# Optimization experiments

Measured on AMD Instinct MI355X. Metric: run time of the kernel, lower is better.

## Reference

```python
import jax, jax.numpy as jnp
import numpy as np

DIM = 1024
HEADS = 16
DIM_HEADS = DIM // HEADS  # 64
DIM_HIDDEN = DIM_HEADS * HEADS


def setup_inputs() -> dict:
    key = jax.random.key(0)
    k1, k2, k3, k4, k5 = jax.random.split(key, 5)
    b, t = 2, 2048
    x = jax.random.normal(k1, (b, t, DIM), dtype=jnp.float32)
    # torch nn.Linear weights are [out_features, in_features]
    s = DIM ** -0.5
    W_q = jax.random.normal(k2, (DIM_HIDDEN, DIM), dtype=jnp.float32) * s
    W_kv = jax.random.normal(k3, (2 * DIM_HIDDEN, DIM), dtype=jnp.float32) * s
    W_out = jax.random.normal(k4, (DIM, DIM_HIDDEN), dtype=jnp.float32) * s
    b_out = jax.random.normal(k5, (DIM,), dtype=jnp.float32) * 0.01
    return {"x": x, "W_q": W_q, "W_kv": W_kv, "W_out": W_out, "b_out": b_out}


def reference(x, W_q, W_kv, W_out, b_out):
    b, t, d = x.shape
    h, e = HEADS, DIM_HEADS
    # projections (Linear: x @ W.T)
    q = jnp.einsum('btd,fd->btf', x, W_q)
    kv = jnp.einsum('btd,fd->btf', x, W_kv)
    k, v = jnp.split(kv, 2, axis=-1)
    # split heads -> (b, h, t, e)
    split = lambda z: z.reshape(b, t, h, e).transpose(0, 2, 1, 3)
    q, k, v = split(q), split(k), split(v)
    # scaled dot-product attention; original uses exp/sum/div softmax
    scores = jnp.einsum('bhqe,bhke->bhqk', q, k) * (e ** -0.5)
    attn = jax.nn.softmax(scores, axis=-1)
    out = jnp.einsum('bhqk,bhke->bhqe', attn, v)
    out = out.transpose(0, 2, 1, 3).reshape(b, t, h * e)
    return jnp.einsum('btf,df->btd', out, W_out) + b_out
```

## Files before the change

kernel.cpp:

```cpp
#include <hip/hip_runtime.h>
#include <hip/hip_bf16.h>

#define BB   2
#define TT   2048
#define DD   1024
#define HH   16
#define EE   64
#define BT   4096

typedef __attribute__((ext_vector_type(8))) short bf16x8;
typedef __attribute__((ext_vector_type(4))) float floatx4;

__device__ __forceinline__ unsigned short f2bf(float f) {
  unsigned int x = __float_as_uint(f);
  x += 0x7fffu + ((x >> 16) & 1u);
  return (unsigned short)(x >> 16);
}
__device__ __forceinline__ uint4 pack8(const float4& a, const float4& b) {
  union { uint4 u; __hip_bfloat162 h[4]; } r;
  r.h[0] = __float22bfloat162_rn(make_float2(a.x, a.y));
  r.h[1] = __float22bfloat162_rn(make_float2(a.z, a.w));
  r.h[2] = __float22bfloat162_rn(make_float2(b.x, b.y));
  r.h[3] = __float22bfloat162_rn(make_float2(b.z, b.w));
  return r.u;
}
__device__ __forceinline__ void ld16(unsigned short* lds, const unsigned short* g) {
  __builtin_amdgcn_global_load_lds(
      (const __attribute__((address_space(1))) unsigned int*)g,
      (__attribute__((address_space(3))) unsigned int*)lds, 16, 0, 0);
}

#define GX   524288
#define GWQ  131072
#define GWKV 262144
#define GWO  131072

__global__ __launch_bounds__(256) void convert_kernel(
    const float* __restrict__ X,  const float* __restrict__ Wq,
    const float* __restrict__ Wkv, const float* __restrict__ Wout,
    unsigned short* __restrict__ Xb, unsigned short* __restrict__ Wb,
    unsigned short* __restrict__ Wob) {
  int g = blockIdx.x * 256 + threadIdx.x;
  const float* src; unsigned short* dst; int gi;
  if (g < GX)                        { src = X;    dst = Xb;  gi = g; }
  else if ((g -= GX) < GWQ)          { src = Wq;   dst = Wb;  gi = g; }
  else if ((g -= GWQ) < GWKV)        { src = Wkv;  dst = Wb + (size_t)GWQ * 8; gi = g; }
  else                               { src = Wout; dst = Wob; gi = g - GWKV; }
  const float4* s4 = reinterpret_cast<const float4*>(src) + (size_t)gi * 2;
  float4 a = s4[0], b = s4[1];
  reinterpret_cast<uint4*>(dst)[gi] = pack8(a, b);
}

__global__ __launch_bounds__(256) void gemm_qkv_mfma(
    const unsigned short* __restrict__ Xb,
    const unsigned short* __restrict__ Wb,
    unsigned short* __restrict__ Qh,
    unsigned short* __restrict__ Kh,
    unsigned short* __restrict__ Vt) {
  __shared__ __align__(16) unsigned short As[128 * 64];
  __shared__ __align__(16) unsigned short Bs[128 * 64];
  const int tid  = threadIdx.x;
  const int lane = tid & 63, w = tid >> 6;
  const int wm = w >> 1, wn = w & 1;
  const int q = lane >> 4, c = lane & 15;
  const int bm0 = blockIdx.y * 128;
  const int bn0 = blockIdx.x * 128;
  const unsigned short* Ag = Xb + (size_t)bm0 * DD;
  const unsigned short* Bg = Wb + (size_t)bn0 * DD;

  floatx4 acc[4][4];
#pragma unroll
  for (int i = 0; i < 4; ++i)
#pragma unroll
    for (int j = 0; j < 4; ++j) acc[i][j] = (floatx4){0.f, 0.f, 0.f, 0.f};

  int prow[4], pch[4];
#pragma unroll
  for (int t = 0; t < 4; ++t) {
    int s = (w * 4 + t) * 64 + lane;
    prow[t] = s >> 3;
    pch[t]  = (s & 7) ^ (prow[t] & 7);
  }
  int aoff[4][2], boff[4][2];
#pragma unroll
  for (int i = 0; i < 4; ++i)
#pragma unroll
    for (int h = 0; h < 2; ++h) {
      aoff[i][h] = (wm * 64 + i * 16 + c) * 64 + (((q + h * 4) ^ (c & 7)) << 3);
      boff[i][h] = (wn * 64 + i * 16 + c) * 64 + (((q + h * 4) ^ (c & 7)) << 3);
    }

  for (int kk = 0; kk < DD; kk += 64) {
    __syncthreads();
#pragma unroll
    for (int t = 0; t < 4; ++t) {
      int i = w * 4 + t;
      ld16(&As[i * 512], &Ag[(size_t)prow[t] * DD + kk + pch[t] * 8]);
      ld16(&Bs[i * 512], &Bg[(size_t)prow[t] * DD + kk + pch[t] * 8]);
    }
    __syncthreads();
    bf16x8 af[4][2], bfr[4][2];
#pragma unroll
    for (int i = 0; i < 4; ++i)
#pragma unroll
      for (int h = 0; h < 2; ++h) {
        af[i][h]  = *reinterpret_cast<const bf16x8*>(&As[aoff[i][h]]);
        bfr[i][h] = *reinterpret_cast<const bf16x8*>(&Bs[boff[i][h]]);
      }
#pragma unroll
    for (int i = 0; i < 4; ++i)
#pragma unroll
      for (int j = 0; j < 4; ++j) {
        acc[i][j] = __builtin_amdgcn_mfma_f32_16x16x32_bf16(af[i][0], bfr[j][0], acc[i][j], 0, 0, 0);
        acc[i][j] = __builtin_amdgcn_mfma_f32_16x16x32_bf16(af[i][1], bfr[j][1], acc[i][j], 0, 0, 0);
      }
  }

  const int region = bn0 >> 10;
#pragma unroll
  for (int i = 0; i < 4; ++i) {
#pragma unroll
    for (int j = 0; j < 4; ++j) {
#pragma unroll
      for (int reg = 0; reg < 4; ++reg) {
        int m = bm0 + wm * 64 + i * 16 + q * 4 + reg;
        int n = bn0 + wn * 64 + j * 16 + c;
        int nb = n & 1023;
        int h = nb >> 6, e = nb & 63;
        int b = m >> 11, t = m & 2047;
        unsigned short v = f2bf(acc[i][j][reg]);
        if (region == 0)      Qh[((size_t)((b * HH + h) * TT + t)) * EE + e] = v;
        else if (region == 1) Kh[((size_t)((b * HH + h) * TT + t)) * EE + e] = v;
        else                  Vt[((size_t)(b * HH + h)) * EE * TT + (size_t)e * TT + t] = v;
      }
    }
  }
}

#define LP 72

__global__ __launch_bounds__(256) void attn_kernel(
    const unsigned short* __restrict__ Qh,
    const unsigned short* __restrict__ Kh,
    const unsigned short* __restrict__ Vtg,
    unsigned short* __restrict__ Aw) {
  __shared__ __align__(16) unsigned short Qs[64 * LP];
  __shared__ __align__(16) unsigned short Ks[64 * LP];
  __shared__ __align__(16) unsigned short Vs[64 * LP];
  __shared__ __align__(16) unsigned short Ps[64 * LP];

  const int tid  = threadIdx.x;
  const int lane = tid & 63;
  const int w    = tid >> 6;
  const int q    = lane >> 4;
  const int c    = lane & 15;
  const int rbase = w * 16;

  const int qt = blockIdx.x;
  const int bh = blockIdx.y;
  const size_t base = (size_t)bh * TT * EE;
  const unsigned short* Qp = Qh + base + (size_t)qt * 64 * EE;
  const unsigned short* Kp = Kh + base;
  const unsigned short* Vp = Vtg + base;

#pragma unroll
  for (int s = 0; s < 2; ++s) {
    int o = tid + s * 256;
    int r = o >> 3, e0 = (o & 7) << 3;
    *reinterpret_cast<uint4*>(&Qs[r * LP + e0]) =
        *reinterpret_cast<const uint4*>(&Qp[(size_t)r * EE + e0]);
  }

  float l_r[4] = {0.f, 0.f, 0.f, 0.f};
  floatx4 o_acc[4];
#pragma unroll
  for (int nt = 0; nt < 4; ++nt) o_acc[nt] = (floatx4){0.f, 0.f, 0.f, 0.f};

  const int a_off = (rbase + c) * LP + q * 8;
  const int b_off = c * LP + q * 8;
  const int p_off = (rbase + q * 4) * LP + c;

  for (int kt = 0; kt < TT / 64; ++kt) {
    __syncthreads();
#pragma unroll
    for (int s = 0; s < 2; ++s) {
      int o = tid + s * 256;
      int r = o >> 3, x0 = (o & 7) << 3;
      *reinterpret_cast<uint4*>(&Ks[r * LP + x0]) =
          *reinterpret_cast<const uint4*>(&Kp[(size_t)(kt * 64 + r) * EE + x0]);
      *reinterpret_cast<uint4*>(&Vs[r * LP + x0]) =
          *reinterpret_cast<const uint4*>(&Vp[(size_t)r * TT + kt * 64 + x0]);
    }
    __syncthreads();

    floatx4 sacc[4];
#pragma unroll
    for (int nt = 0; nt < 4; ++nt) sacc[nt] = (floatx4){0.f, 0.f, 0.f, 0.f};
    bf16x8 aq0 = *reinterpret_cast<const bf16x8*>(&Qs[a_off]);
    bf16x8 aq1 = *reinterpret_cast<const bf16x8*>(&Qs[a_off + 32]);
#pragma unroll
    for (int nt = 0; nt < 4; ++nt) {
      bf16x8 bk0 = *reinterpret_cast<const bf16x8*>(&Ks[b_off + nt * 16 * LP]);
      bf16x8 bk1 = *reinterpret_cast<const bf16x8*>(&Ks[b_off + nt * 16 * LP + 32]);
      sacc[nt] = __builtin_amdgcn_mfma_f32_16x16x32_bf16(aq0, bk0, sacc[nt], 0, 0, 0);
      sacc[nt] = __builtin_amdgcn_mfma_f32_16x16x32_bf16(aq1, bk1, sacc[nt], 0, 0, 0);
    }

#pragma unroll
    for (int nt = 0; nt < 4; ++nt)
#pragma unroll
      for (int reg = 0; reg < 4; ++reg) {
        float p = __expf(sacc[nt][reg] * 0.125f);
        l_r[reg] += p;
        Ps[p_off + reg * LP + nt * 16] = f2bf(p);
      }

    __syncthreads();

    bf16x8 ap0 = *reinterpret_cast<const bf16x8*>(&Ps[a_off]);
    bf16x8 ap1 = *reinterpret_cast<const bf16x8*>(&Ps[a_off + 32]);
#pragma unroll
    for (int nt = 0; nt < 4; ++nt) {
      bf16x8 bv0 = *reinterpret_cast<const bf16x8*>(&Vs[b_off + nt * 16 * LP]);
      bf16x8 bv1 = *reinterpret_cast<const bf16x8*>(&Vs[b_off + nt * 16 * LP + 32]);
      o_acc[nt] = __builtin_amdgcn_mfma_f32_16x16x32_bf16(ap0, bv0, o_acc[nt], 0, 0, 0);
      o_acc[nt] = __builtin_amdgcn_mfma_f32_16x16x32_bf16(ap1, bv1, o_acc[nt], 0, 0, 0);
    }
  }

#pragma unroll
  for (int reg = 0; reg < 4; ++reg)
#pragma unroll
    for (int mask = 1; mask < 16; mask <<= 1)
      l_r[reg] += __shfl_xor(l_r[reg], mask, 64);

  const int b = bh >> 4, h = bh & 15;
#pragma unroll
  for (int reg = 0; reg < 4; ++reg) {
    int t = qt * 64 + rbase + q * 4 + reg;
    float inv = 1.0f / l_r[reg];
    size_t rowoff = ((size_t)(b * TT + t)) * DD + h * EE;
#pragma unroll
    for (int nt = 0; nt < 4; ++nt)
      Aw[rowoff + nt * 16 + c] = f2bf(o_acc[nt][reg] * inv);
  }
}

__global__ __launch_bounds__(256) void gemm_out_mfma(
    const unsigned short* __restrict__ A,
    const unsigned short* __restrict__ Wob,
    const float* __restrict__ bias,
    float* __restrict__ out) {
  __shared__ __align__(16) unsigned short As[128 * 64];
  __shared__ __align__(16) unsigned short Bs[64 * 64];
  const int tid  = threadIdx.x;
  const int lane = tid & 63, w = tid >> 6;
  const int wm = w >> 1, wn = w & 1;
  const int q = lane >> 4, c = lane & 15;
  const int bm0 = blockIdx.y * 128;
  const int bn0 = blockIdx.x * 64;
  const unsigned short* Ag = A + (size_t)bm0 * DD;
  const unsigned short* Bg = Wob + (size_t)bn0 * DD;

  floatx4 acc[4][2];
#pragma unroll
  for (int i = 0; i < 4; ++i)
#pragma unroll
    for (int j = 0; j < 2; ++j) acc[i][j] = (floatx4){0.f, 0.f, 0.f, 0.f};

  int parow[4], pach[4];
#pragma unroll
  for (int t = 0; t < 4; ++t) {
    int s = (w * 4 + t) * 64 + lane;
    parow[t] = s >> 3;
    pach[t]  = (s & 7) ^ (parow[t] & 7);
  }
  int pbrow[2], pbch[2];
#pragma unroll
  for (int t = 0; t < 2; ++t) {
    int s = (w * 2 + t) * 64 + lane;
    pbrow[t] = s >> 3;
    pbch[t]  = (s & 7) ^ (pbrow[t] & 7);
  }

  for (int kk = 0; kk < DD; kk += 64) {
    __syncthreads();
#pragma unroll
    for (int t = 0; t < 4; ++t)
      ld16(&As[(w * 4 + t) * 512], &Ag[(size_t)parow[t] * DD + kk + pach[t] * 8]);
#pragma unroll
    for (int t = 0; t < 2; ++t)
      ld16(&Bs[(w * 2 + t) * 512], &Bg[(size_t)pbrow[t] * DD + kk + pbch[t] * 8]);
    __syncthreads();
    bf16x8 af[4][2], bfr[2][2];
#pragma unroll
    for (int h = 0; h < 2; ++h) {
      int ksw = ((q + h * 4) ^ (c & 7)) << 3;
#pragma unroll
      for (int i = 0; i < 4; ++i)
        af[i][h] = *reinterpret_cast<const bf16x8*>(&As[(wm * 64 + i * 16 + c) * 64 + ksw]);
#pragma unroll
      for (int j = 0; j < 2; ++j)
        bfr[j][h] = *reinterpret_cast<const bf16x8*>(&Bs[(wn * 32 + j * 16 + c) * 64 + ksw]);
    }
#pragma unroll
    for (int i = 0; i < 4; ++i)
#pragma unroll
      for (int j = 0; j < 2; ++j) {
        acc[i][j] = __builtin_amdgcn_mfma_f32_16x16x32_bf16(af[i][0], bfr[j][0], acc[i][j], 0, 0, 0);
        acc[i][j] = __builtin_amdgcn_mfma_f32_16x16x32_bf16(af[i][1], bfr[j][1], acc[i][j], 0, 0, 0);
      }
  }

#pragma unroll
  for (int i = 0; i < 4; ++i) {
#pragma unroll
    for (int j = 0; j < 2; ++j) {
      int n = bn0 + wn * 32 + j * 16 + c;
      float bv = bias[n];
#pragma unroll
      for (int reg = 0; reg < 4; ++reg) {
        int m = bm0 + wm * 64 + i * 16 + q * 4 + reg;
        out[(size_t)m * DD + n] = acc[i][j][reg] + bv;
      }
    }
  }
}

extern "C" void kernel_launch(void* const* d_in, const int* in_sizes, int n_in,
                              void* d_out, int out_size, void* d_ws, size_t ws_size,
                              hipStream_t stream) {
  const float* X    = (const float*)d_in[0];
  const float* Wq   = (const float*)d_in[1];
  const float* Wkv  = (const float*)d_in[2];
  const float* Wout = (const float*)d_in[3];
  const float* bout = (const float*)d_in[4];
  float* out = (float*)d_out;

  unsigned short* Qh  = (unsigned short*)d_ws;
  unsigned short* Kh  = Qh + (size_t)BT * DD;
  unsigned short* Vt  = Kh + (size_t)BT * DD;
  unsigned short* Aw  = Vt + (size_t)BT * DD;
  unsigned short* Xb  = Aw;
  unsigned short* Wb  = Aw + (size_t)BT * DD;
  unsigned short* Wob = Wb + (size_t)3 * 1024 * DD;

  convert_kernel<<<dim3(4096), 256, 0, stream>>>(X, Wq, Wkv, Wout, Xb, Wb, Wob);
  gemm_qkv_mfma<<<dim3(24, 32), 256, 0, stream>>>(Xb, Wb, Qh, Kh, Vt);
  attn_kernel<<<dim3(32, 32), 256, 0, stream>>>(Qh, Kh, Vt, Aw);
  gemm_out_mfma<<<dim3(16, 32), 256, 0, stream>>>(Aw, Wob, bout, out);
}
```

Baseline: 232.3 us.

## Transpose S via swapped MFMA operands, reuse Q LDS for P, fold scale into projection

```diff
diff --git a/kernel.cpp b/kernel.cpp
--- a/kernel.cpp
+++ b/kernel.cpp
@@ -15,6 +15,11 @@
   unsigned int x = __float_as_uint(f);
   x += 0x7fffu + ((x >> 16) & 1u);
   return (unsigned short)(x >> 16);
+}
+__device__ __forceinline__ unsigned int pack2u(float a, float b) {
+  union { __hip_bfloat162 h; unsigned int u; } r;
+  r.h = __float22bfloat162_rn(make_float2(a, b));
+  return r.u;
 }
 __device__ __forceinline__ uint4 pack8(const float4& a, const float4& b) {
   union { uint4 u; __hip_bfloat162 h[4]; } r;
@@ -117,6 +122,7 @@
   }
 
   const int region = bn0 >> 10;
+  const float scl = (region == 0) ? 0.125f : 1.0f;
 #pragma unroll
   for (int i = 0; i < 4; ++i) {
 #pragma unroll
@@ -128,7 +134,7 @@
         int nb = n & 1023;
         int h = nb >> 6, e = nb & 63;
         int b = m >> 11, t = m & 2047;
-        unsigned short v = f2bf(acc[i][j][reg]);
+        unsigned short v = f2bf(acc[i][j][reg] * scl);
         if (region == 0)      Qh[((size_t)((b * HH + h) * TT + t)) * EE + e] = v;
         else if (region == 1) Kh[((size_t)((b * HH + h) * TT + t)) * EE + e] = v;
         else                  Vt[((size_t)(b * HH + h)) * EE * TT + (size_t)e * TT + t] = v;
@@ -147,7 +153,6 @@
   __shared__ __align__(16) unsigned short Qs[64 * LP];
   __shared__ __align__(16) unsigned short Ks[64 * LP];
   __shared__ __align__(16) unsigned short Vs[64 * LP];
-  __shared__ __align__(16) unsigned short Ps[64 * LP];
 
   const int tid  = threadIdx.x;
   const int lane = tid & 63;
@@ -170,15 +175,17 @@
     *reinterpret_cast<uint4*>(&Qs[r * LP + e0]) =
         *reinterpret_cast<const uint4*>(&Qp[(size_t)r * EE + e0]);
   }
-
-  float l_r[4] = {0.f, 0.f, 0.f, 0.f};
-  floatx4 o_acc[4];
-#pragma unroll
-  for (int nt = 0; nt < 4; ++nt) o_acc[nt] = (floatx4){0.f, 0.f, 0.f, 0.f};
+  __syncthreads();
 
   const int a_off = (rbase + c) * LP + q * 8;
   const int b_off = c * LP + q * 8;
-  const int p_off = (rbase + q * 4) * LP + c;
+  const bf16x8 aq0 = *reinterpret_cast<const bf16x8*>(&Qs[a_off]);
+  const bf16x8 aq1 = *reinterpret_cast<const bf16x8*>(&Qs[a_off + 32]);
+
+  float l_sum = 0.0f;
+  floatx4 o_acc[4];
+#pragma unroll
+  for (int nt = 0; nt < 4; ++nt) o_acc[nt] = (floatx4){0.f, 0.f, 0.f, 0.f};
 
   for (int kt = 0; kt < TT / 64; ++kt) {
     __syncthreads();
@@ -195,30 +202,30 @@
 
     floatx4 sacc[4];
 #pragma unroll
-    for (int nt = 0; nt < 4; ++nt) sacc[nt] = (floatx4){0.f, 0.f, 0.f, 0.f};
-    bf16x8 aq0 = *reinterpret_cast<const bf16x8*>(&Qs[a_off]);
-    bf16x8 aq1 = *reinterpret_cast<const bf16x8*>(&Qs[a_off + 32]);
-#pragma unroll
     for (int nt = 0; nt < 4; ++nt) {
       bf16x8 bk0 = *reinterpret_cast<const bf16x8*>(&Ks[b_off + nt * 16 * LP]);
       bf16x8 bk1 = *reinterpret_cast<const bf16x8*>(&Ks[b_off + nt * 16 * LP + 32]);
-      sacc[nt] = __builtin_amdgcn_mfma_f32_16x16x32_bf16(aq0, bk0, sacc[nt], 0, 0, 0);
-      sacc[nt] = __builtin_amdgcn_mfma_f32_16x16x32_bf16(aq1, bk1, sacc[nt], 0, 0, 0);
-    }
-
-#pragma unroll
-    for (int nt = 0; nt < 4; ++nt)
-#pragma unroll
-      for (int reg = 0; reg < 4; ++reg) {
-        float p = __expf(sacc[nt][reg] * 0.125f);
-        l_r[reg] += p;
-        Ps[p_off + reg * LP + nt * 16] = f2bf(p);
-      }
-
-    __syncthreads();
-
-    bf16x8 ap0 = *reinterpret_cast<const bf16x8*>(&Ps[a_off]);
-    bf16x8 ap1 = *reinterpret_cast<const bf16x8*>(&Ps[a_off + 32]);
+      sacc[nt] = (floatx4){0.f, 0.f, 0.f, 0.f};
+      sacc[nt] = __builtin_amdgcn_mfma_f32_16x16x32_bf16(bk0, aq0, sacc[nt], 0, 0, 0);
+      sacc[nt] = __builtin_amdgcn_mfma_f32_16x16x32_bf16(bk1, aq1, sacc[nt], 0, 0, 0);
+    }
+
+#pragma unroll
+    for (int nt = 0; nt < 4; ++nt) {
+      float p0 = __expf(sacc[nt][0]);
+      float p1 = __expf(sacc[nt][1]);
+      float p2 = __expf(sacc[nt][2]);
+      float p3 = __expf(sacc[nt][3]);
+      l_sum += (p0 + p1) + (p2 + p3);
+      uint2 pk;
+      pk.x = pack2u(p0, p1);
+      pk.y = pack2u(p2, p3);
+      *reinterpret_cast<uint2*>(&Qs[(rbase + c) * LP + nt * 16 + q * 4]) = pk;
+    }
+    asm volatile("s_waitcnt lgkmcnt(0)" ::: "memory");
+
+    bf16x8 ap0 = *reinterpret_cast<const bf16x8*>(&Qs[a_off]);
+    bf16x8 ap1 = *reinterpret_cast<const bf16x8*>(&Qs[a_off + 32]);
 #pragma unroll
     for (int nt = 0; nt < 4; ++nt) {
       bf16x8 bv0 = *reinterpret_cast<const bf16x8*>(&Vs[b_off + nt * 16 * LP]);
@@ -228,21 +235,21 @@
     }
   }
 
+  l_sum += __shfl_xor(l_sum, 16, 64);
+  l_sum += __shfl_xor(l_sum, 32, 64);
+  float linv[4];
 #pragma unroll
   for (int reg = 0; reg < 4; ++reg)
-#pragma unroll
-    for (int mask = 1; mask < 16; mask <<= 1)
-      l_r[reg] += __shfl_xor(l_r[reg], mask, 64);
+    linv[reg] = 1.0f / __shfl(l_sum, q * 4 + reg, 64);
 
   const int b = bh >> 4, h = bh & 15;
 #pragma unroll
   for (int reg = 0; reg < 4; ++reg) {
     int t = qt * 64 + rbase + q * 4 + reg;
-    float inv = 1.0f / l_r[reg];
     size_t rowoff = ((size_t)(b * TT + t)) * DD + h * EE;
 #pragma unroll
     for (int nt = 0; nt < 4; ++nt)
-      Aw[rowoff + nt * 16 + c] = f2bf(o_acc[nt][reg] * inv);
+      Aw[rowoff + nt * 16 + c] = f2bf(o_acc[nt][reg] * linv[reg]);
   }
 }
 
```

After: 209.6 us. 9.8% less time.
